# Kernel tuning notes

Measured on AMD Instinct MI355X. Metric: run time of the kernel, lower is better.

## Reference

```python
import jax, jax.numpy as jnp
import numpy as np

DT = 0.01  # constructor dt
T = 8_388_608  # number of timesteps


def setup_inputs() -> dict:
    key = jax.random.key(0)
    k1, k2 = jax.random.split(key)
    initial_state = jax.random.normal(k1, (1, 2), dtype=jnp.float32)
    actions = jax.random.normal(k2, (T, 1), dtype=jnp.float32)
    mass = jnp.float32(5.0)            # nn.Parameter init
    friction_coeff = jnp.float32(0.5)  # nn.Parameter init
    return {
        "initial_state": initial_state,
        "actions": actions,
        "mass": mass,
        "friction_coeff": friction_coeff,
    }


def reference(initial_state, actions, mass, friction_coeff):
    # Euler integration of 1D kinematics, rolled out with lax.scan
    # state: [1, 2] = [position, velocity]; actions: [T, 1]
    m_safe = jnp.abs(mass) + 0.001

    def step(state, action):
        x, v = state[:, 0], state[:, 1]
        F_applied = action  # [1]
        F_net = F_applied - friction_coeff * v
        a = F_net / m_safe
        v_next = v + a * DT
        x_next = x + v_next * DT
        s = jnp.stack([x_next, v_next], axis=1)  # [1, 2]
        return s, s

    _, traj = jax.lax.scan(step, initial_state, actions[:, 0][:, None])
    # traj: [T, 1, 2]; concatenate initial state like torch.cat(states, dim=0)
    states = jnp.concatenate([initial_state[None], traj], axis=0)  # [T+1, 1, 2]
    return states.reshape(-1, 2)  # [(T+1), 2]
```

## Files before the change

### kernel.cpp

```cpp
#include <hip/hip_runtime.h>
#include <math.h>


#define TPB 256
#define SEGT 16
#define TILES 2
#define TILE_STEPS (TPB * SEGT)
#define BLOCK_STEPS (TILE_STEPS * TILES)
#define GPT 4
#define POISON64 0xAAAAAAAAAAAAAAAAull
#define SLOT 8

union F2U { unsigned long long u; float2 f; };

__device__ __forceinline__ double ipow_d(double a, int n) {
    double r = 1.0, b = a;
    while (n) { if (n & 1) r *= b; b *= b; n >>= 1; }
    return r;
}

__device__ __forceinline__ double cgeom(double alpha, double An, int n) {
    const double DTd = (double)0.01f;
    double den = 1.0 - alpha;
    if (fabs(den) < 1e-12) return DTd * (double)n;
    return DTd * alpha * (1.0 - An) / den;
}

__global__ __launch_bounds__(TPB, 4) void k_fused(
        const float* __restrict__ act,
        unsigned long long* aggU,
        unsigned long long* preU,
        const float* __restrict__ init,
        const float* __restrict__ mp,
        const float* __restrict__ fp,
        float2* __restrict__ out2,
        int nBlocks)
{
    __shared__ float4 sOut[TPB * 8];
    __shared__ float2 sBP;
    double* sA = (double*)sOut;
    double* sB = sA + TPB;
    double* sC = sB + TPB;
    double* sD = sC + TPB;

    const int t = threadIdx.x;
    const int b = blockIdx.x;

    const float m_safe = fabsf(mp[0]) + 0.001f;
    const float fric   = fp[0];
    const float DTf    = 0.01f;
    const float beta   = DTf / m_safe;
    const float alpha  = 1.0f - fric * beta;

    const double ad  = 1.0 - (double)fric * ((double)0.01f) / (double)m_safe;
    const double A16 = ipow_d(ad, SEGT);
    const double C16 = cgeom(ad, A16, SEGT);
    const double A4k = ipow_d(ad, TILE_STEPS);
    const double C4k = cgeom(ad, A4k, TILE_STEPS);
    const double A8k = A4k * A4k;
    const double C8k = C4k + C4k * A4k;

    float4 actv[TILES][4];
#pragma unroll
    for (int k = 0; k < TILES; ++k) {
        const float4* p = (const float4*)(act + (size_t)b * BLOCK_STEPS
                                          + k * TILE_STEPS + t * SEGT);
        actv[k][0] = p[0]; actv[k][1] = p[1]; actv[k][2] = p[2]; actv[k][3] = p[3];
    }

    float preA[TILES], preB[TILES], preC[TILES], preD[TILES];
    double tB0 = 0.0, tD0 = 0.0, tB1 = 0.0, tD1 = 0.0;
#pragma unroll
    for (int k = 0; k < TILES; ++k) {
        float v = 0.0f, x = 0.0f;
#pragma unroll
        for (int q = 0; q < 4; ++q) {
            float4 a = actv[k][q];
            v = fmaf(alpha, v, beta * a.x); x = fmaf(v, DTf, x);
            v = fmaf(alpha, v, beta * a.y); x = fmaf(v, DTf, x);
            v = fmaf(alpha, v, beta * a.z); x = fmaf(v, DTf, x);
            v = fmaf(alpha, v, beta * a.w); x = fmaf(v, DTf, x);
        }
        if (k > 0) __syncthreads();
        sA[t] = A16; sB[t] = (double)v; sC[t] = C16; sD[t] = (double)x;
        __syncthreads();
        for (int d = 1; d < TPB; d <<= 1) {
            double a1, b1, c1, d1, a2, b2, c2, d2;
            const bool p = (t >= d);
            if (p) {
                a1 = sA[t-d]; b1 = sB[t-d]; c1 = sC[t-d]; d1 = sD[t-d];
                a2 = sA[t];   b2 = sB[t];   c2 = sC[t];   d2 = sD[t];
            }
            __syncthreads();
            if (p) {
                sA[t] = a2 * a1;
                sB[t] = fma(a2, b1, b2);
                sC[t] = fma(c2, a1, c1);
                sD[t] = fma(c2, b1, d1 + d2);
            }
            __syncthreads();
        }
        if (t == 0) { preA[k] = 1.f; preB[k] = 0.f; preC[k] = 0.f; preD[k] = 0.f; }
        else {
            preA[k] = (float)sA[t-1]; preB[k] = (float)sB[t-1];
            preC[k] = (float)sC[t-1]; preD[k] = (float)sD[t-1];
        }
        const double tb = sB[TPB-1], td = sD[TPB-1];
        if (k == 0) { tB0 = tb; tD0 = td; } else { tB1 = tb; tD1 = td; }
    }

    const double bB = fma(A4k, tB0, tB1);
    const double bD = tD0 + C4k * tB0 + tD1;
    if (t == 0) {
        F2U u; u.f = make_float2((float)bB, (float)bD);
        atomicExch(&aggU[(size_t)b * SLOT], u.u);
    }

    if (b == 0) {
        double eB[GPT], eD[GPT];
        double cA = 1.0, cB = 0.0, cC = 0.0, cD = 0.0;
#pragma unroll
        for (int i = 0; i < GPT; ++i) {
            const int blk = GPT * t + i;
            F2U u;
            u.u = atomicCAS(&aggU[(size_t)blk * SLOT], POISON64, POISON64);
            while (u.u == POISON64) {
                __builtin_amdgcn_s_sleep(2);
                u.u = atomicCAS(&aggU[(size_t)blk * SLOT], POISON64, POISON64);
            }
            eB[i] = (double)u.f.x; eD[i] = (double)u.f.y;
            double nA = A8k * cA;
            double nB = fma(A8k, cB, eB[i]);
            double nC = cC + C8k * cA;
            double nD = cD + C8k * cB + eD[i];
            cA = nA; cB = nB; cC = nC; cD = nD;
        }
        __syncthreads();
        sA[t] = cA; sB[t] = cB; sC[t] = cC; sD[t] = cD;
        __syncthreads();
        for (int d = 1; d < TPB; d <<= 1) {
            double a1, b1, c1, d1, a2, b2, c2, d2;
            const bool p = (t >= d);
            if (p) {
                a1 = sA[t-d]; b1 = sB[t-d]; c1 = sC[t-d]; d1 = sD[t-d];
                a2 = sA[t];   b2 = sB[t];   c2 = sC[t];   d2 = sD[t];
            }
            __syncthreads();
            if (p) {
                sA[t] = a2 * a1;
                sB[t] = fma(a2, b1, b2);
                sC[t] = fma(c2, a1, c1);
                sD[t] = fma(c2, b1, d1 + d2);
            }
            __syncthreads();
        }
        double pA, pB, pC, pD;
        if (t == 0) { pA = 1.0; pB = 0.0; pC = 0.0; pD = 0.0; }
        else        { pA = sA[t-1]; pB = sB[t-1]; pC = sC[t-1]; pD = sD[t-1]; }

        const double v0 = (double)init[1];
        const double x0 = (double)init[0];
#pragma unroll
        for (int i = 0; i < GPT; ++i) {
            F2U u;
            u.f = make_float2((float)fma(pA, v0, pB),
                              (float)(x0 + pC * v0 + pD));
            atomicExch(&preU[(size_t)(GPT * t + i) * SLOT], u.u);
            double nA = A8k * pA;
            double nB = fma(A8k, pB, eB[i]);
            double nC = pC + C8k * pA;
            double nD = pD + C8k * pB + eD[i];
            pA = nA; pB = nB; pC = nC; pD = nD;
        }
        if (t == 0) sBP = make_float2((float)v0, (float)x0);
        __syncthreads();
    } else {
        if (t == 0) {
            F2U u;
            u.u = atomicCAS(&preU[(size_t)b * SLOT], POISON64, POISON64);
            while (u.u == POISON64) {
                __builtin_amdgcn_s_sleep(8);
                u.u = atomicCAS(&preU[(size_t)b * SLOT], POISON64, POISON64);
            }
            sBP = u.f;
        }
        __syncthreads();
    }

    const float2 bp = sBP;
    double vtile = (double)bp.x, xtile = (double)bp.y;

#pragma unroll
    for (int k = 0; k < TILES; ++k) {
        const float vt = (float)vtile, xt = (float)xtile;
        float v = fmaf(preA[k], vt, preB[k]);
        float x = xt + preC[k] * vt + preD[k];

        float4* so = &sOut[t * 8];
        const int sw = t & 7;
#pragma unroll
        for (int q = 0; q < 4; ++q) {
            float4 a = actv[k][q];
            float4 e0, e1;
            e0.x = x; e0.y = v;
            v = fmaf(alpha, v, beta * a.x); x = fmaf(v, DTf, x);
            e0.z = x; e0.w = v;
            v = fmaf(alpha, v, beta * a.y); x = fmaf(v, DTf, x);
            e1.x = x; e1.y = v;
            v = fmaf(alpha, v, beta * a.z); x = fmaf(v, DTf, x);
            e1.z = x; e1.w = v;
            v = fmaf(alpha, v, beta * a.w); x = fmaf(v, DTf, x);
            so[(2 * q)     ^ sw] = e0;
            so[(2 * q + 1) ^ sw] = e1;
        }
        if (k == TILES - 1 && b == nBlocks - 1 && t == TPB - 1)
            out2[(size_t)nBlocks * BLOCK_STEPS] = make_float2(x, v);

        __syncthreads();
        float4* o4 = (float4*)out2 + ((size_t)b * BLOCK_STEPS + k * TILE_STEPS) / 2;
#pragma unroll
        for (int it = 0; it < 8; ++it) {
            const int j = t + it * TPB;
            const int src = (j & ~7) | ((j & 7) ^ ((j >> 3) & 7));
            o4[j] = sOut[src];
        }
        if (k + 1 < TILES) {
            const double nv = fma(A4k, vtile, tB0);
            const double nx = xtile + C4k * vtile + tD0;
            vtile = nv; xtile = nx;
            __syncthreads();
        }
    }
}

extern "C" void kernel_launch(void* const* d_in, const int* in_sizes, int n_in,
                              void* d_out, int out_size, void* d_ws, size_t ws_size,
                              hipStream_t stream) {
    const float* init    = (const float*)d_in[0];
    const float* actions = (const float*)d_in[1];
    const float* mass    = (const float*)d_in[2];
    const float* fric    = (const float*)d_in[3];

    const int T = in_sizes[1];
    const int nBlocks = T / BLOCK_STEPS;

    unsigned long long* aggU = (unsigned long long*)d_ws;
    unsigned long long* preU = aggU + (size_t)nBlocks * SLOT;

    k_fused<<<nBlocks, TPB, 0, stream>>>(actions, aggU, preU, init, mass, fric,
                                         (float2*)d_out, nBlocks);
}
```

Before: 109.7 us.

## Replace shared-memory Hillis-Steele scans with wavefront shuffle scans

The block-level affine prefix scans, both the per-tile one and block 0's cross-block one, now run as 64-lane wavefront shuffle scans on the (B,D) components. The A and C coefficients are computed analytically per lane, and a small serial combine across the 4 waves goes through shared memory. This removes the many __syncthreads and LDS round trips of the 8-step shared-memory scan, and both tiles are scanned together. Block 0 also polls its 4 aggregate slots in an interleaved way instead of one at a time. The cost is more double-precision arithmetic per lane and a small reordering of floating-point operations.

After: 111.4 us. No clear change (+1.5%).

```diff
diff --git a/kernel.cpp b/kernel.cpp
--- a/kernel.cpp
+++ b/kernel.cpp
@@ -19,10 +19,10 @@
     return r;
 }
 
-__device__ __forceinline__ double cgeom(double alpha, double An, int n) {
+__device__ __forceinline__ double cgeom(double alpha, double An, double n) {
     const double DTd = (double)0.01f;
     double den = 1.0 - alpha;
-    if (fabs(den) < 1e-12) return DTd * (double)n;
+    if (fabs(den) < 1e-12) return DTd * n;
     return DTd * alpha * (1.0 - An) / den;
 }
 
@@ -38,13 +38,12 @@
 {
     __shared__ float4 sOut[TPB * 8];
     __shared__ float2 sBP;
-    double* sA = (double*)sOut;
-    double* sB = sA + TPB;
-    double* sC = sB + TPB;
-    double* sD = sC + TPB;
+    double* sW = (double*)sOut;
 
     const int t = threadIdx.x;
     const int b = blockIdx.x;
+    const int l = t & 63;
+    const int w = t >> 6;
 
     const float m_safe = fabsf(mp[0]) + 0.001f;
     const float fric   = fp[0];
@@ -54,9 +53,9 @@
 
     const double ad  = 1.0 - (double)fric * ((double)0.01f) / (double)m_safe;
     const double A16 = ipow_d(ad, SEGT);
-    const double C16 = cgeom(ad, A16, SEGT);
+    const double C16 = cgeom(ad, A16, (double)SEGT);
     const double A4k = ipow_d(ad, TILE_STEPS);
-    const double C4k = cgeom(ad, A4k, TILE_STEPS);
+    const double C4k = cgeom(ad, A4k, (double)TILE_STEPS);
     const double A8k = A4k * A4k;
     const double C8k = C4k + C4k * A4k;
 
@@ -68,8 +67,7 @@
         actv[k][0] = p[0]; actv[k][1] = p[1]; actv[k][2] = p[2]; actv[k][3] = p[3];
     }
 
-    float preA[TILES], preB[TILES], preC[TILES], preD[TILES];
-    double tB0 = 0.0, tD0 = 0.0, tB1 = 0.0, tD1 = 0.0;
+    float vs[TILES], xs[TILES];
 #pragma unroll
     for (int k = 0; k < TILES; ++k) {
         float v = 0.0f, x = 0.0f;
@@ -81,82 +79,122 @@
             v = fmaf(alpha, v, beta * a.z); x = fmaf(v, DTf, x);
             v = fmaf(alpha, v, beta * a.w); x = fmaf(v, DTf, x);
         }
-        if (k > 0) __syncthreads();
-        sA[t] = A16; sB[t] = (double)v; sC[t] = C16; sD[t] = (double)x;
-        __syncthreads();
-        for (int d = 1; d < TPB; d <<= 1) {
-            double a1, b1, c1, d1, a2, b2, c2, d2;
-            const bool p = (t >= d);
-            if (p) {
-                a1 = sA[t-d]; b1 = sB[t-d]; c1 = sC[t-d]; d1 = sD[t-d];
-                a2 = sA[t];   b2 = sB[t];   c2 = sC[t];   d2 = sD[t];
-            }
-            __syncthreads();
-            if (p) {
-                sA[t] = a2 * a1;
-                sB[t] = fma(a2, b1, b2);
-                sC[t] = fma(c2, a1, c1);
-                sD[t] = fma(c2, b1, d1 + d2);
-            }
-            __syncthreads();
-        }
-        if (t == 0) { preA[k] = 1.f; preB[k] = 0.f; preC[k] = 0.f; preD[k] = 0.f; }
-        else {
-            preA[k] = (float)sA[t-1]; preB[k] = (float)sB[t-1];
-            preC[k] = (float)sC[t-1]; preD[k] = (float)sD[t-1];
-        }
-        const double tb = sB[TPB-1], td = sD[TPB-1];
-        if (k == 0) { tB0 = tb; tD0 = td; } else { tB1 = tb; tD1 = td; }
-    }
-
-    const double bB = fma(A4k, tB0, tB1);
-    const double bD = tD0 + C4k * tB0 + tD1;
+        vs[k] = v; xs[k] = x;
+    }
+
+    double b0 = (double)vs[0], d0 = (double)xs[0];
+    double b1 = (double)vs[1], d1 = (double)xs[1];
+    double Ar = A16, Cr = C16;
+    double Al = 1.0, Cl = 0.0;
+#pragma unroll
+    for (int r = 0; r < 6; ++r) {
+        const int m = 1 << r;
+        double bu0 = __shfl_up(b0, m); double du0 = __shfl_up(d0, m);
+        double bu1 = __shfl_up(b1, m); double du1 = __shfl_up(d1, m);
+        if (l >= m) {
+            d0 = du0 + Cr * bu0 + d0;  b0 = Ar * bu0 + b0;
+            d1 = du1 + Cr * bu1 + d1;  b1 = Ar * bu1 + b1;
+        }
+        if (l & m) { Cl = Cl + Cr * Al; Al = Ar * Al; }
+        Cr = Cr * (1.0 + Ar); Ar = Ar * Ar;
+    }
+    const double A64 = Ar, C64 = Cr;
+    double bx0 = __shfl_up(b0, 1), dx0 = __shfl_up(d0, 1);
+    double bx1 = __shfl_up(b1, 1), dx1 = __shfl_up(d1, 1);
+
+    if (l == 63) {
+        sW[w * 2]     = b0; sW[w * 2 + 1]     = d0;
+        sW[8 + w * 2] = b1; sW[8 + w * 2 + 1] = d1;
+    }
+    __syncthreads();
+
+    double Bw0 = 0.0, Dw0 = 0.0, Bw1 = 0.0, Dw1 = 0.0;
+    double tb0 = 0.0, td0 = 0.0, tb1 = 0.0, td1 = 0.0;
+#pragma unroll
+    for (int j = 0; j < 4; ++j) {
+        if (j == w) { Bw0 = tb0; Dw0 = td0; Bw1 = tb1; Dw1 = td1; }
+        double wb0 = sW[j * 2],     wd0 = sW[j * 2 + 1];
+        double wb1 = sW[8 + j * 2], wd1 = sW[8 + j * 2 + 1];
+        td0 = td0 + C64 * tb0 + wd0;  tb0 = A64 * tb0 + wb0;
+        td1 = td1 + C64 * tb1 + wd1;  tb1 = A64 * tb1 + wb1;
+    }
+
+    const double bB = A4k * tb0 + tb1;
+    const double bD = td0 + C4k * tb0 + td1;
     if (t == 0) {
         F2U u; u.f = make_float2((float)bB, (float)bD);
         atomicExch(&aggU[(size_t)b * SLOT], u.u);
     }
 
+    double Awp = 1.0, Cwp = 0.0;
+#pragma unroll
+    for (int j = 0; j < 3; ++j) if (j < w) { Cwp = Cwp + C64 * Awp; Awp = A64 * Awp; }
+    const float preAf = (float)(Al * Awp);
+    const float preCf = (float)(Cwp + Cl * Awp);
+    float preBf[TILES], preDf[TILES];
+    {
+        double pb0, pd0, pb1, pd1;
+        if (l == 0) { pb0 = Bw0; pd0 = Dw0; pb1 = Bw1; pd1 = Dw1; }
+        else {
+            pb0 = Al * Bw0 + bx0;  pd0 = Dw0 + Cl * Bw0 + dx0;
+            pb1 = Al * Bw1 + bx1;  pd1 = Dw1 + Cl * Bw1 + dx1;
+        }
+        preBf[0] = (float)pb0; preDf[0] = (float)pd0;
+        preBf[1] = (float)pb1; preDf[1] = (float)pd1;
+    }
+
     if (b == 0) {
         double eB[GPT], eD[GPT];
-        double cA = 1.0, cB = 0.0, cC = 0.0, cD = 0.0;
-#pragma unroll
-        for (int i = 0; i < GPT; ++i) {
-            const int blk = GPT * t + i;
-            F2U u;
-            u.u = atomicCAS(&aggU[(size_t)blk * SLOT], POISON64, POISON64);
-            while (u.u == POISON64) {
-                __builtin_amdgcn_s_sleep(2);
-                u.u = atomicCAS(&aggU[(size_t)blk * SLOT], POISON64, POISON64);
+        {
+            F2U uv[GPT];
+            int rem = (1 << GPT) - 1;
+            while (rem) {
+#pragma unroll
+                for (int i = 0; i < GPT; ++i) if (rem & (1 << i)) {
+                    F2U u;
+                    u.u = atomicCAS(&aggU[(size_t)(GPT * t + i) * SLOT], POISON64, POISON64);
+                    if (u.u != POISON64) { uv[i] = u; rem &= ~(1 << i); }
+                }
+                if (rem) __builtin_amdgcn_s_sleep(2);
             }
-            eB[i] = (double)u.f.x; eD[i] = (double)u.f.y;
-            double nA = A8k * cA;
-            double nB = fma(A8k, cB, eB[i]);
-            double nC = cC + C8k * cA;
-            double nD = cD + C8k * cB + eD[i];
-            cA = nA; cB = nB; cC = nC; cD = nD;
-        }
-        __syncthreads();
-        sA[t] = cA; sB[t] = cB; sC[t] = cC; sD[t] = cD;
-        __syncthreads();
-        for (int d = 1; d < TPB; d <<= 1) {
-            double a1, b1, c1, d1, a2, b2, c2, d2;
-            const bool p = (t >= d);
-            if (p) {
-                a1 = sA[t-d]; b1 = sB[t-d]; c1 = sC[t-d]; d1 = sD[t-d];
-                a2 = sA[t];   b2 = sB[t];   c2 = sC[t];   d2 = sD[t];
-            }
-            __syncthreads();
-            if (p) {
-                sA[t] = a2 * a1;
-                sB[t] = fma(a2, b1, b2);
-                sC[t] = fma(c2, a1, c1);
-                sD[t] = fma(c2, b1, d1 + d2);
-            }
-            __syncthreads();
-        }
-        double pA, pB, pC, pD;
-        if (t == 0) { pA = 1.0; pB = 0.0; pC = 0.0; pD = 0.0; }
-        else        { pA = sA[t-1]; pB = sB[t-1]; pC = sC[t-1]; pD = sD[t-1]; }
+#pragma unroll
+            for (int i = 0; i < GPT; ++i) { eB[i] = (double)uv[i].f.x; eD[i] = (double)uv[i].f.y; }
+        }
+        double cB = 0.0, cD = 0.0;
+#pragma unroll
+        for (int i = 0; i < GPT; ++i) { cD = cD + C8k * cB + eD[i]; cB = A8k * cB + eB[i]; }
+
+        double Ab2 = A8k * A8k,  Cb2 = C8k * (1.0 + A8k);
+        double Arg = Ab2 * Ab2,  Crg = Cb2 * (1.0 + Ab2);
+        double Alg = 1.0, Clg = 0.0;
+        double gb = cB, gd = cD;
+#pragma unroll
+        for (int r = 0; r < 6; ++r) {
+            const int m = 1 << r;
+            double bu = __shfl_up(gb, m), du = __shfl_up(gd, m);
+            if (l >= m) { gd = du + Crg * bu + gd; gb = Arg * bu + gb; }
+            if (l & m) { Clg = Clg + Crg * Alg; Alg = Arg * Alg; }
+            Crg = Crg * (1.0 + Arg); Arg = Arg * Arg;
+        }
+        const double AG64 = Arg, CG64 = Crg;
+        double gbx = __shfl_up(gb, 1), gdx = __shfl_up(gd, 1);
+        if (l == 63) { sW[16 + w * 2] = gb; sW[16 + w * 2 + 1] = gd; }
+        __syncthreads();
+        double Bwg = 0.0, Dwg = 0.0, accb = 0.0, accd = 0.0;
+#pragma unroll
+        for (int j = 0; j < 4; ++j) {
+            if (j == w) { Bwg = accb; Dwg = accd; }
+            double wb = sW[16 + j * 2], wd = sW[16 + j * 2 + 1];
+            accd = accd + CG64 * accb + wd;  accb = AG64 * accb + wb;
+        }
+        double Awg = 1.0, Cwg = 0.0;
+#pragma unroll
+        for (int j = 0; j < 3; ++j) if (j < w) { Cwg = Cwg + CG64 * Awg; Awg = AG64 * Awg; }
+        double pA = Alg * Awg;
+        double pC = Cwg + Clg * Awg;
+        double pB, pD;
+        if (l == 0) { pB = Bwg; pD = Dwg; }
+        else { pB = Alg * Bwg + gbx; pD = Dwg + Clg * Bwg + gdx; }
 
         const double v0 = (double)init[1];
         const double x0 = (double)init[0];
@@ -166,10 +204,10 @@
             u.f = make_float2((float)fma(pA, v0, pB),
                               (float)(x0 + pC * v0 + pD));
             atomicExch(&preU[(size_t)(GPT * t + i) * SLOT], u.u);
+            double nD = pD + C8k * pB + eD[i];
+            double nB = A8k * pB + eB[i];
+            double nC = pC + C8k * pA;
             double nA = A8k * pA;
-            double nB = fma(A8k, pB, eB[i]);
-            double nC = pC + C8k * pA;
-            double nD = pD + C8k * pB + eD[i];
             pA = nA; pB = nB; pC = nC; pD = nD;
         }
         if (t == 0) sBP = make_float2((float)v0, (float)x0);
@@ -193,8 +231,8 @@
 #pragma unroll
     for (int k = 0; k < TILES; ++k) {
         const float vt = (float)vtile, xt = (float)xtile;
-        float v = fmaf(preA[k], vt, preB[k]);
-        float x = xt + preC[k] * vt + preD[k];
+        float v = fmaf(preAf, vt, preBf[k]);
+        float x = xt + preCf * vt + preDf[k];
 
         float4* so = &sOut[t * 8];
         const int sw = t & 7;
@@ -225,8 +263,8 @@
             o4[j] = sOut[src];
         }
         if (k + 1 < TILES) {
-            const double nv = fma(A4k, vtile, tB0);
-            const double nx = xtile + C4k * vtile + tD0;
+            const double nv = fma(A4k, vtile, tb0);
+            const double nx = xtile + C4k * vtile + td0;
             vtile = nv; xtile = nx;
             __syncthreads();
         }
```
